# Performance work log

Hardware: AMD Instinct MI355X
Metric: run time of the kernel (lower is better)

## Reference

```python
import jax, jax.numpy as jnp
import numpy as np

B, Q_LOG, Q_PHYS, E = 32, 256, 256, 4096

def setup_inputs() -> dict:
    key = jax.random.key(0)
    k1, k2, k3, k4, k5 = jax.random.split(key, 5)
    P = jax.nn.softmax(jax.random.normal(k1, (B, Q_LOG, Q_PHYS), dtype=jnp.float32), axis=-1)
    # hop distances in [0, 10); d_swap = 3*max(d_hw-1, 0) so some entries are zero
    d_hw = jax.random.uniform(k2, (Q_PHYS, Q_PHYS), dtype=jnp.float32, maxval=10.0)
    edge_i = jax.random.randint(k3, (E,), 0, Q_LOG, dtype=jnp.int32)
    edge_j = jax.random.randint(k4, (E,), 0, Q_LOG, dtype=jnp.int32)
    edge_weights = jax.random.uniform(k5, (E,), dtype=jnp.float32, minval=0.1, maxval=5.0)
    return {"P": P, "d_hw": d_hw, "edge_i": edge_i, "edge_j": edge_j,
            "edge_weights": edge_weights}

def reference(P, d_hw, edge_i, edge_j, edge_weights):
    # d_swap(p,q) = 3 * max(d_hop(p,q) - 1, 0); normalize=False
    d_swap = 3.0 * jnp.maximum(d_hw - 1.0, 0.0)          # [Q,Q]
    Pi = P[:, edge_i, :]                                  # [B,E,Q]
    Pj = P[:, edge_j, :]                                  # [B,E,Q]
    # cost_be = sum_{p,q} Pi[b,e,p] d_swap[p,q] Pj[b,e,q]
    cost = jnp.einsum('bep,pq,beq->be', Pi, d_swap, Pj)   # [B,E]
    per_edge = cost.mean(axis=0)                          # mean over batch, per edge
    total_w = jnp.maximum(edge_weights.sum(), 1e-8)
    return (edge_weights * per_edge).sum() / total_w
```

## Files before the change

kernel.cpp:

```cpp
#include <hip/hip_runtime.h>
#include <hip/hip_bf16.h>

#define NB   32
#define NQ   256
#define NE   4096
#define MROWS (NB * NQ)

typedef __attribute__((ext_vector_type(8))) short short8;
typedef __attribute__((ext_vector_type(4))) float f32x4;

#define MFMA(a, b, c) __builtin_amdgcn_mfma_f32_16x16x32_bf16((a), (b), (c), 0, 0, 0)

__device__ ushort g_Pbf[MROWS * NQ];
__device__ ushort g_Mbf[MROWS * NQ];
__device__ ushort g_DbfT[NQ * NQ];
__device__ float  g_Ct[NB * NQ * NQ];
__device__ float  g_edge_val[NE];

__device__ __forceinline__ ushort f2bf(float f) {
    unsigned u = __float_as_uint(f);
    u += 0x7fffu + ((u >> 16) & 1u);
    return (ushort)(u >> 16);
}

__global__ __launch_bounds__(256) void prep_kernel(const float* __restrict__ P,
                                                   const float* __restrict__ d_hw) {
    const int b = blockIdx.x;
    const int tid = threadIdx.x;
    if (b < 512) {
        const int gid = b * 256 + tid;
        const float4* Pv = (const float4*)P;
#pragma unroll
        for (int it = 0; it < 4; ++it) {
            const int i = gid + it * (512 * 256);
            float4 v = Pv[i];
            ushort4 o;
            o.x = f2bf(v.x); o.y = f2bf(v.y); o.z = f2bf(v.z); o.w = f2bf(v.w);
            ((ushort4*)g_Pbf)[i] = o;
        }
    } else {
        const int p0 = (b - 512) * 16;
#pragma unroll
        for (int pr = 0; pr < 16; ++pr) {
            const int p = p0 + pr;
            float d = d_hw[p * NQ + tid];
            float s = d > 1.f ? 3.f * (d - 1.f) : 0.f;
            g_DbfT[tid * NQ + p] = f2bf(s);
        }
    }
}

__global__ __launch_bounds__(256) void gemm1_kernel() {
    const int tid = threadIdx.x;
    const int wave = tid >> 6, lane = tid & 63;
    const int l15 = lane & 15, koff = (lane >> 4) * 8;
    const int rowBase = blockIdx.y * 64 + (wave >> 1) * 32;
    const int colBase = blockIdx.x * 64 + (wave & 1) * 32;

    const ushort* A0 = g_Pbf + (rowBase + l15) * NQ + koff;
    const ushort* A1 = A0 + 16 * NQ;
    const ushort* B0 = g_DbfT + (colBase + l15) * NQ + koff;
    const ushort* B1 = B0 + 16 * NQ;

    f32x4 acc00 = {0,0,0,0}, acc01 = {0,0,0,0}, acc10 = {0,0,0,0}, acc11 = {0,0,0,0};
#pragma unroll 4
    for (int k0 = 0; k0 < NQ; k0 += 32) {
        short8 a0 = *(const short8*)(A0 + k0);
        short8 a1 = *(const short8*)(A1 + k0);
        short8 b0 = *(const short8*)(B0 + k0);
        short8 b1 = *(const short8*)(B1 + k0);
        acc00 = MFMA(a0, b0, acc00);
        acc01 = MFMA(a0, b1, acc01);
        acc10 = MFMA(a1, b0, acc10);
        acc11 = MFMA(a1, b1, acc11);
    }

    const int orow = (lane >> 4) * 4;
#pragma unroll
    for (int i = 0; i < 4; ++i) {
        g_Mbf[(rowBase + orow + i) * NQ + colBase + l15]           = f2bf(acc00[i]);
        g_Mbf[(rowBase + orow + i) * NQ + colBase + 16 + l15]      = f2bf(acc01[i]);
        g_Mbf[(rowBase + 16 + orow + i) * NQ + colBase + l15]      = f2bf(acc10[i]);
        g_Mbf[(rowBase + 16 + orow + i) * NQ + colBase + 16 + l15] = f2bf(acc11[i]);
    }
}

__global__ __launch_bounds__(256) void gemm2_kernel() {
    const int b = blockIdx.z;
    const int tid = threadIdx.x;
    const int wave = tid >> 6, lane = tid & 63;
    const int l15 = lane & 15, koff = (lane >> 4) * 8;
    const int iBase = blockIdx.y * 64 + (wave >> 1) * 32;
    const int jBase = blockIdx.x * 64 + (wave & 1) * 32;

    const ushort* A0 = g_Mbf + (b * NQ + iBase + l15) * NQ + koff;
    const ushort* A1 = A0 + 16 * NQ;
    const ushort* B0 = g_Pbf + (b * NQ + jBase + l15) * NQ + koff;
    const ushort* B1 = B0 + 16 * NQ;

    f32x4 acc00 = {0,0,0,0}, acc01 = {0,0,0,0}, acc10 = {0,0,0,0}, acc11 = {0,0,0,0};
#pragma unroll 4
    for (int k0 = 0; k0 < NQ; k0 += 32) {
        short8 a0 = *(const short8*)(A0 + k0);
        short8 a1 = *(const short8*)(A1 + k0);
        short8 b0 = *(const short8*)(B0 + k0);
        short8 b1 = *(const short8*)(B1 + k0);
        acc00 = MFMA(a0, b0, acc00);
        acc01 = MFMA(a0, b1, acc01);
        acc10 = MFMA(a1, b0, acc10);
        acc11 = MFMA(a1, b1, acc11);
    }

    const int orow = (lane >> 4) * 4;
    float* Cb = g_Ct + b * (NQ * NQ);
    *(f32x4*)&Cb[(jBase + l15) * NQ + iBase + orow]           = acc00;
    *(f32x4*)&Cb[(jBase + 16 + l15) * NQ + iBase + orow]      = acc01;
    *(f32x4*)&Cb[(jBase + l15) * NQ + iBase + 16 + orow]      = acc10;
    *(f32x4*)&Cb[(jBase + 16 + l15) * NQ + iBase + 16 + orow] = acc11;
}

__global__ __launch_bounds__(256) void edge_gather_kernel(const int* __restrict__ edge_i,
                                                          const int* __restrict__ edge_j,
                                                          const float* __restrict__ edge_w) {
    const int e = blockIdx.x * 256 + threadIdx.x;
    const int i = edge_i[e];
    const int j = edge_j[e];
    const int base = j * NQ + i;
    float s = 0.f;
#pragma unroll
    for (int b = 0; b < NB; ++b) s += g_Ct[b * (NQ * NQ) + base];
    g_edge_val[e] = edge_w[e] * (s * (1.0f / NB));
}

__global__ __launch_bounds__(256) void finalize_kernel(const float* __restrict__ edge_w,
                                                       float* __restrict__ out) {
    const int tid = threadIdx.x;
    float num = 0.f, den = 0.f;
    for (int e = tid; e < NE; e += 256) {
        num += g_edge_val[e];
        den += edge_w[e];
    }
#pragma unroll
    for (int off = 32; off > 0; off >>= 1) {
        num += __shfl_down(num, off);
        den += __shfl_down(den, off);
    }
    __shared__ float pn[4], pd[4];
    const int wid = tid >> 6;
    if ((tid & 63) == 0) { pn[wid] = num; pd[wid] = den; }
    __syncthreads();
    if (tid == 0) {
        float n = pn[0] + pn[1] + pn[2] + pn[3];
        float d = pd[0] + pd[1] + pd[2] + pd[3];
        d = d > 1e-8f ? d : 1e-8f;
        out[0] = n / d;
    }
}

extern "C" void kernel_launch(void* const* d_in, const int* in_sizes, int n_in,
                              void* d_out, int out_size, void* d_ws, size_t ws_size,
                              hipStream_t stream) {
    const float* P      = (const float*)d_in[0];
    const float* d_hw   = (const float*)d_in[1];
    const int*   edge_i = (const int*)d_in[2];
    const int*   edge_j = (const int*)d_in[3];
    const float* edge_w = (const float*)d_in[4];
    float* out = (float*)d_out;

    prep_kernel<<<528, 256, 0, stream>>>(P, d_hw);
    gemm1_kernel<<<dim3(4, 128), 256, 0, stream>>>();
    gemm2_kernel<<<dim3(4, 4, NB), 256, 0, stream>>>();
    edge_gather_kernel<<<NE / 256, 256, 0, stream>>>(edge_i, edge_j, edge_w);
    finalize_kernel<<<1, 256, 0, stream>>>(edge_w, out);
}
```

Before: 49.55 us.

## Fuse bf16 conversion into GEMMs and merge gather with finalize via last-block reduction

```diff
diff --git a/kernel.cpp b/kernel.cpp
--- a/kernel.cpp
+++ b/kernel.cpp
@@ -11,64 +11,66 @@
 
 #define MFMA(a, b, c) __builtin_amdgcn_mfma_f32_16x16x32_bf16((a), (b), (c), 0, 0, 0)
 
-__device__ ushort g_Pbf[MROWS * NQ];
 __device__ ushort g_Mbf[MROWS * NQ];
-__device__ ushort g_DbfT[NQ * NQ];
 __device__ float  g_Ct[NB * NQ * NQ];
 __device__ float  g_edge_val[NE];
+__device__ int    g_arrive = 0;
+
+__device__ __forceinline__ short8 cvt8(float4 u0, float4 u1) {
+    short8 s;
+    s[0] = (short)__bfloat16_as_ushort(__float2bfloat16(u0.x));
+    s[1] = (short)__bfloat16_as_ushort(__float2bfloat16(u0.y));
+    s[2] = (short)__bfloat16_as_ushort(__float2bfloat16(u0.z));
+    s[3] = (short)__bfloat16_as_ushort(__float2bfloat16(u0.w));
+    s[4] = (short)__bfloat16_as_ushort(__float2bfloat16(u1.x));
+    s[5] = (short)__bfloat16_as_ushort(__float2bfloat16(u1.y));
+    s[6] = (short)__bfloat16_as_ushort(__float2bfloat16(u1.z));
+    s[7] = (short)__bfloat16_as_ushort(__float2bfloat16(u1.w));
+    return s;
+}
 
 __device__ __forceinline__ ushort f2bf(float f) {
-    unsigned u = __float_as_uint(f);
-    u += 0x7fffu + ((u >> 16) & 1u);
-    return (ushort)(u >> 16);
+    return __bfloat16_as_ushort(__float2bfloat16(f));
 }
 
-__global__ __launch_bounds__(256) void prep_kernel(const float* __restrict__ P,
-                                                   const float* __restrict__ d_hw) {
-    const int b = blockIdx.x;
+__global__ __launch_bounds__(256) void gemm1_kernel(const float* __restrict__ P,
+                                                    const float* __restrict__ d_hw) {
+    __shared__ ushort Ds[64][264];
+
     const int tid = threadIdx.x;
-    if (b < 512) {
-        const int gid = b * 256 + tid;
-        const float4* Pv = (const float4*)P;
+    const int colBase = blockIdx.x * 64;
+    const int rowBase = blockIdx.y * 64;
+
+    {
+        const int c4 = (tid & 15) * 4;
+        const int kr = tid >> 4;
 #pragma unroll
-        for (int it = 0; it < 4; ++it) {
-            const int i = gid + it * (512 * 256);
-            float4 v = Pv[i];
-            ushort4 o;
-            o.x = f2bf(v.x); o.y = f2bf(v.y); o.z = f2bf(v.z); o.w = f2bf(v.w);
-            ((ushort4*)g_Pbf)[i] = o;
-        }
-    } else {
-        const int p0 = (b - 512) * 16;
-#pragma unroll
-        for (int pr = 0; pr < 16; ++pr) {
-            const int p = p0 + pr;
-            float d = d_hw[p * NQ + tid];
-            float s = d > 1.f ? 3.f * (d - 1.f) : 0.f;
-            g_DbfT[tid * NQ + p] = f2bf(s);
+        for (int p = 0; p < 16; ++p) {
+            const int k = kr + p * 16;
+            float4 v = *(const float4*)&d_hw[k * NQ + colBase + c4];
+            Ds[c4 + 0][k] = f2bf(v.x > 1.f ? 3.f * (v.x - 1.f) : 0.f);
+            Ds[c4 + 1][k] = f2bf(v.y > 1.f ? 3.f * (v.y - 1.f) : 0.f);
+            Ds[c4 + 2][k] = f2bf(v.z > 1.f ? 3.f * (v.z - 1.f) : 0.f);
+            Ds[c4 + 3][k] = f2bf(v.w > 1.f ? 3.f * (v.w - 1.f) : 0.f);
         }
     }
-}
+    __syncthreads();
 
-__global__ __launch_bounds__(256) void gemm1_kernel() {
-    const int tid = threadIdx.x;
     const int wave = tid >> 6, lane = tid & 63;
     const int l15 = lane & 15, koff = (lane >> 4) * 8;
-    const int rowBase = blockIdx.y * 64 + (wave >> 1) * 32;
-    const int colBase = blockIdx.x * 64 + (wave & 1) * 32;
+    const int rBase = rowBase + (wave >> 1) * 32;
+    const int cLoc  = (wave & 1) * 32 + l15;
 
-    const ushort* A0 = g_Pbf + (rowBase + l15) * NQ + koff;
-    const ushort* A1 = A0 + 16 * NQ;
-    const ushort* B0 = g_DbfT + (colBase + l15) * NQ + koff;
-    const ushort* B1 = B0 + 16 * NQ;
+    const float* A0 = P + (rBase + l15) * NQ + koff;
+    const float* A1 = A0 + 16 * NQ;
 
     f32x4 acc00 = {0,0,0,0}, acc01 = {0,0,0,0}, acc10 = {0,0,0,0}, acc11 = {0,0,0,0};
-#pragma unroll 4
+#pragma unroll
     for (int k0 = 0; k0 < NQ; k0 += 32) {
-        short8 a0 = *(const short8*)(A0 + k0);
-        short8 a1 = *(const short8*)(A1 + k0);
-        short8 b0 = *(const short8*)(B0 + k0);
-        short8 b1 = *(const short8*)(B1 + k0);
+        short8 a0 = cvt8(*(const float4*)(A0 + k0), *(const float4*)(A0 + k0 + 4));
+        short8 a1 = cvt8(*(const float4*)(A1 + k0), *(const float4*)(A1 + k0 + 4));
+        short8 b0 = *(const short8*)&Ds[cLoc][koff + k0];
+        short8 b1 = *(const short8*)&Ds[cLoc + 16][koff + k0];
         acc00 = MFMA(a0, b0, acc00);
         acc01 = MFMA(a0, b1, acc01);
         acc10 = MFMA(a1, b0, acc10);
@@ -76,16 +78,17 @@
     }
 
     const int orow = (lane >> 4) * 4;
+    const int cBase = colBase + (wave & 1) * 32 + l15;
 #pragma unroll
     for (int i = 0; i < 4; ++i) {
-        g_Mbf[(rowBase + orow + i) * NQ + colBase + l15]           = f2bf(acc00[i]);
-        g_Mbf[(rowBase + orow + i) * NQ + colBase + 16 + l15]      = f2bf(acc01[i]);
-        g_Mbf[(rowBase + 16 + orow + i) * NQ + colBase + l15]      = f2bf(acc10[i]);
-        g_Mbf[(rowBase + 16 + orow + i) * NQ + colBase + 16 + l15] = f2bf(acc11[i]);
+        g_Mbf[(rBase + orow + i) * NQ + cBase]           = f2bf(acc00[i]);
+        g_Mbf[(rBase + orow + i) * NQ + cBase + 16]      = f2bf(acc01[i]);
+        g_Mbf[(rBase + 16 + orow + i) * NQ + cBase]      = f2bf(acc10[i]);
+        g_Mbf[(rBase + 16 + orow + i) * NQ + cBase + 16] = f2bf(acc11[i]);
     }
 }
 
-__global__ __launch_bounds__(256) void gemm2_kernel() {
+__global__ __launch_bounds__(256) void gemm2_kernel(const float* __restrict__ P) {
     const int b = blockIdx.z;
     const int tid = threadIdx.x;
     const int wave = tid >> 6, lane = tid & 63;
@@ -95,16 +98,16 @@
 
     const ushort* A0 = g_Mbf + (b * NQ + iBase + l15) * NQ + koff;
     const ushort* A1 = A0 + 16 * NQ;
-    const ushort* B0 = g_Pbf + (b * NQ + jBase + l15) * NQ + koff;
-    const ushort* B1 = B0 + 16 * NQ;
+    const float*  B0 = P + (b * NQ + jBase + l15) * NQ + koff;
+    const float*  B1 = B0 + 16 * NQ;
 
     f32x4 acc00 = {0,0,0,0}, acc01 = {0,0,0,0}, acc10 = {0,0,0,0}, acc11 = {0,0,0,0};
-#pragma unroll 4
+#pragma unroll
     for (int k0 = 0; k0 < NQ; k0 += 32) {
         short8 a0 = *(const short8*)(A0 + k0);
         short8 a1 = *(const short8*)(A1 + k0);
-        short8 b0 = *(const short8*)(B0 + k0);
-        short8 b1 = *(const short8*)(B1 + k0);
+        short8 b0 = cvt8(*(const float4*)(B0 + k0), *(const float4*)(B0 + k0 + 4));
+        short8 b1 = cvt8(*(const float4*)(B1 + k0), *(const float4*)(B1 + k0 + 4));
         acc00 = MFMA(a0, b0, acc00);
         acc01 = MFMA(a0, b1, acc01);
         acc10 = MFMA(a1, b0, acc10);
@@ -119,26 +122,37 @@
     *(f32x4*)&Cb[(jBase + 16 + l15) * NQ + iBase + 16 + orow] = acc11;
 }
 
-__global__ __launch_bounds__(256) void edge_gather_kernel(const int* __restrict__ edge_i,
-                                                          const int* __restrict__ edge_j,
-                                                          const float* __restrict__ edge_w) {
-    const int e = blockIdx.x * 256 + threadIdx.x;
+__global__ __launch_bounds__(256) void gather_final_kernel(const int* __restrict__ edge_i,
+                                                           const int* __restrict__ edge_j,
+                                                           const float* __restrict__ edge_w,
+                                                           float* __restrict__ out) {
+    const int tid = threadIdx.x;
+    const int e = blockIdx.x * 8 + (tid >> 5);
+    const int b = tid & 31;
+
     const int i = edge_i[e];
     const int j = edge_j[e];
-    const int base = j * NQ + i;
-    float s = 0.f;
+    float v = g_Ct[b * (NQ * NQ) + j * NQ + i];
+
 #pragma unroll
-    for (int b = 0; b < NB; ++b) s += g_Ct[b * (NQ * NQ) + base];
-    g_edge_val[e] = edge_w[e] * (s * (1.0f / NB));
-}
+    for (int off = 16; off > 0; off >>= 1) v += __shfl_down(v, off, 32);
+    if (b == 0) g_edge_val[e] = edge_w[e] * (v * (1.0f / NB));
 
-__global__ __launch_bounds__(256) void finalize_kernel(const float* __restrict__ edge_w,
-                                                       float* __restrict__ out) {
-    const int tid = threadIdx.x;
+    __threadfence();
+    __syncthreads();
+    __shared__ int s_last;
+    if (tid == 0) {
+        int old = atomicAdd(&g_arrive, 1);
+        s_last = ((old & 511) == 511);
+    }
+    __syncthreads();
+    if (!s_last) return;
+    __threadfence();
+
     float num = 0.f, den = 0.f;
-    for (int e = tid; e < NE; e += 256) {
-        num += g_edge_val[e];
-        den += edge_w[e];
+    for (int e2 = tid; e2 < NE; e2 += 256) {
+        num += g_edge_val[e2];
+        den += edge_w[e2];
     }
 #pragma unroll
     for (int off = 32; off > 0; off >>= 1) {
@@ -167,9 +181,7 @@
     const float* edge_w = (const float*)d_in[4];
     float* out = (float*)d_out;
 
-    prep_kernel<<<528, 256, 0, stream>>>(P, d_hw);
-    gemm1_kernel<<<dim3(4, 128), 256, 0, stream>>>();
-    gemm2_kernel<<<dim3(4, 4, NB), 256, 0, stream>>>();
-    edge_gather_kernel<<<NE / 256, 256, 0, stream>>>(edge_i, edge_j, edge_w);
-    finalize_kernel<<<1, 256, 0, stream>>>(edge_w, out);
+    gemm1_kernel<<<dim3(4, 128), 256, 0, stream>>>(P, d_hw);
+    gemm2_kernel<<<dim3(4, 4, NB), 256, 0, stream>>>(P);
+    gather_final_kernel<<<512, 256, 0, stream>>>(edge_i, edge_j, edge_w, out);
 }
```

After: 73.61 us. +48.6%, slower.
